# Performance work log

Hardware: AMD Instinct MI355X
Metric: run time of the kernel (lower is better)

The kernel has to match this reference:

```python
import jax, jax.numpy as jnp
import numpy as np

C_S, C_HID, H, P, V = 128, 16, 12, 4, 8
EPS = 1e-08
SOFTPLUS_INV_1 = 0.541324854612918


def _pts_from_linear(x, n_pts):
    # torch: split [..., 3*n] into 3 chunks of n, stack on dim=-1 -> [..., n, 3]
    B, N = x.shape[:2]
    return jnp.moveaxis(x.reshape(B, N, 3, n_pts), -2, -1)


def setup_inputs() -> dict:
    key = jax.random.key(0)
    ks = jax.random.split(key, 16)
    B, N = 2, 512
    hc = H * C_HID            # 192
    hpq = H * P * 3           # 144
    hpkv = H * (P + V) * 3    # 432
    cat_dim = H * (C_HID + V * 4)  # 576
    sc = 0.02
    inp = {
        "s": jax.random.normal(ks[0], (B, N, C_S), jnp.float32),
        "R": jax.random.normal(ks[1], (B, N, 3, 3), jnp.float32),
        "t": jax.random.normal(ks[2], (B, N, 3), jnp.float32),
        "pair_mask": jnp.ones((B, N, N), jnp.float32),
        "Wq": jax.random.normal(ks[3], (C_S, hc), jnp.float32) * sc,
        "bq": jnp.zeros((hc,), jnp.float32),
        "Wkv": jax.random.normal(ks[4], (C_S, 2 * hc), jnp.float32) * sc,
        "bkv": jnp.zeros((2 * hc,), jnp.float32),
        "Wqp": jax.random.normal(ks[5], (C_S, hpq), jnp.float32) * sc,
        "bqp": jnp.zeros((hpq,), jnp.float32),
        "Wkvp": jax.random.normal(ks[6], (C_S, hpkv), jnp.float32) * sc,
        "bkvp": jnp.zeros((hpkv,), jnp.float32),
        "head_weights": jnp.full((H,), SOFTPLUS_INV_1, jnp.float32),
        "Wout": jax.random.normal(ks[7], (cat_dim, C_S), jnp.float32) * sc,
        "bout": jnp.zeros((C_S,), jnp.float32),
    }
    return inp


def reference(s, R, t, pair_mask, Wq, bq, Wkv, bkv, Wqp, bqp, Wkvp, bkvp,
              head_weights, Wout, bout):
    B, N, _ = s.shape
    # scalar q/k/v
    q = (s @ Wq + bq).reshape(B, N, H, C_HID)
    kv = (s @ Wkv + bkv).reshape(B, N, H, 2 * C_HID)
    k, v = kv[..., :C_HID], kv[..., C_HID:]

    # point q/k/v in global frame: R x + t
    qp = _pts_from_linear(s @ Wqp + bqp, H * P)           # [B,N,HP,3]
    qp = jnp.einsum('bnij,bnpj->bnpi', R, qp) + t[:, :, None]
    qp = qp.reshape(B, N, H, P, 3)
    kvp = _pts_from_linear(s @ Wkvp + bkvp, H * (P + V))  # [B,N,H(P+V),3]
    kvp = jnp.einsum('bnij,bnpj->bnpi', R, kvp) + t[:, :, None]
    kvp = kvp.reshape(B, N, H, P + V, 3)
    kp, vp = kvp[..., :P, :], kvp[..., P:, :]

    # scalar attention logits [B,H,N,N]
    a = jnp.einsum('bihc,bjhc->bhij', q, k) * (1.0 / np.sqrt(3 * C_HID))

    # point-distance bias: sum_p ||q_i - k_j||^2 via |q|^2+|k|^2-2q.k
    sq_q = jnp.sum(qp * qp, axis=(-1, -2))   # [B,N,H]
    sq_k = jnp.sum(kp * kp, axis=(-1, -2))   # [B,N,H]
    cross = jnp.einsum('bihpc,bjhpc->bhij', qp, kp)
    d2 = (jnp.swapaxes(sq_q, 1, 2)[..., :, None]
          + jnp.swapaxes(sq_k, 1, 2)[..., None, :]
          - 2.0 * cross)                      # [B,H,N,N]
    hw = jax.nn.softplus(head_weights) * np.sqrt(1.0 / (3 * (P * 9.0 / 2)))
    pt_att = d2 * hw[None, :, None, None] * (-0.5)

    square_mask = 100000.0 * (pair_mask - 1.0)            # [B,N,N]
    a = jax.nn.softmax(a + pt_att + square_mask[:, None], axis=-1)

    # scalar output
    o = jnp.einsum('bhij,bjhc->bihc', a, v).reshape(B, N, H * C_HID)

    # point output, rotated back to local frame: R^T (x - t) form -> R^T x - t
    o_pt = jnp.einsum('bhij,bjhvc->bihvc', a, vp)         # [B,N,H,V,3]
    o_pt = jnp.einsum('bnji,bnhvj->bnhvi', R, o_pt) - t[:, :, None, None]
    o_pt_norm = jnp.sqrt(jnp.sum(o_pt * o_pt, axis=-1) + EPS).reshape(B, N, H * V)
    o_pt_flat = o_pt.reshape(B, N, H * V, 3)

    cat = jnp.concatenate(
        [o, o_pt_flat[..., 0], o_pt_flat[..., 1], o_pt_flat[..., 2], o_pt_norm],
        axis=-1)                                           # [B,N,576]
    return cat @ Wout + bout
```

## Files before the change

kernel.cpp:

```cpp
#include <hip/hip_runtime.h>
#include <hip/hip_bf16.h>
#include <math.h>

#define H_    12
#define B_    2
#define N_    512
#define BH_   (B_*H_)
#define QSCALE 0.14433756729740643f
#define CPT_K  0.13608276348795434f

#define OFF_WPP  1245184
#define OFF_WOP  1318912
#define OFF_BIA  1355776
#define OFF_QB   1356928
#define OFF_KP   1553536
#define OFF_VP   1750144
#define OFF_SA   2045056
#define OFF_SB   2057344
#define OFF_CATP 2069632

typedef __attribute__((ext_vector_type(8))) short sh8;
typedef __attribute__((ext_vector_type(4))) float f32x4;
typedef unsigned short u16t;

static __device__ __forceinline__ u16t f2b(float x) {
    __hip_bfloat16 h = __float2bfloat16(x);
    return *reinterpret_cast<u16t*>(&h);
}
static __device__ __forceinline__ int catp_idx(int tok, int col) {
    return (tok >> 4)*9216 + (col >> 5)*512 + ((col >> 3) & 3)*128
         + (tok & 15)*8 + (col & 7);
}

__global__ __launch_bounds__(256) void convert_kernel(
    const float* __restrict__ Wq,  const float* __restrict__ bq,
    const float* __restrict__ Wkv, const float* __restrict__ bkv,
    const float* __restrict__ Wqp, const float* __restrict__ bqp,
    const float* __restrict__ Wkvp,const float* __restrict__ bkvp,
    const float* __restrict__ Wout, float* __restrict__ ws)
{
    const int g = blockIdx.x * 256 + threadIdx.x;
    union { sh8 v; u16t u[8]; } pk;

    if (g < 18432) {
        int u = g;
        int n = u & 63, kq = (u >> 6) & 3, ks = (u >> 8) & 3, nt = u >> 10;
        int col = nt*64 + n, k0 = ks*32 + kq*8;
        const float* w; int lc, od;
        if (col < 192)      { w = Wq;   lc = col;     od = 192; }
        else if (col < 576) { w = Wkv;  lc = col-192; od = 384; }
        else if (col < 720) { w = Wqp;  lc = col-576; od = 144; }
        else                { w = Wkvp; lc = col-720; od = 432; }
        #pragma unroll
        for (int j = 0; j < 8; ++j) pk.u[j] = f2b(w[(k0+j)*od + lc]);
        *((sh8*)((u16t*)(ws + OFF_WPP)) + u) = pk.v;
    } else if (g < 27648) {
        int u = g - 18432;
        int n = u & 63, kq = (u >> 6) & 3, rem = u >> 8;
        int ks = rem % 18, nt = rem / 18;
        int col = nt*64 + n, k0 = ks*32 + kq*8;
        #pragma unroll
        for (int j = 0; j < 8; ++j) pk.u[j] = f2b(Wout[(k0+j)*128 + col]);
        *((sh8*)((u16t*)(ws + OFF_WOP)) + u) = pk.v;
    } else if (g < 28800) {
        int col = g - 27648;
        float bv;
        if (col < 192)      bv = bq[col];
        else if (col < 576) bv = bkv[col-192];
        else if (col < 720) bv = bqp[col-576];
        else                bv = bkvp[col-720];
        ws[OFF_BIA + col] = bv;
    }
}

__global__ __launch_bounds__(512) void projpack_kernel(
    const float* __restrict__ s,
    const float* __restrict__ Rg, const float* __restrict__ tg,
    const float* __restrict__ hwg, float* __restrict__ ws)
{
    __shared__ float ldsP[8][1160];

    u16t* Qb = (u16t*)(ws + OFF_QB);
    u16t* Kp = (u16t*)(ws + OFF_KP);
    u16t* Vp = (u16t*)(ws + OFF_VP);
    float* sa_g = ws + OFF_SA;
    float* sb_g = ws + OFF_SB;

    const int tid  = threadIdx.x;
    const int w    = tid >> 6, lane = tid & 63;
    const int kq   = lane >> 4, lx = lane & 15;
    const int tok0 = blockIdx.x * 8;
    const int b    = tok0 >> 9, n0 = tok0 & 511;

    sh8 afr[4];
    #pragma unroll
    for (int ks = 0; ks < 4; ++ks) {
        const float* src = s + (tok0 + (lx & 7))*128 + ks*32 + kq*8;
        float4 u0 = *(const float4*)(src);
        float4 u1 = *(const float4*)(src+4);
        union { sh8 v; u16t u[8]; } pk;
        pk.u[0]=f2b(u0.x); pk.u[1]=f2b(u0.y); pk.u[2]=f2b(u0.z); pk.u[3]=f2b(u0.w);
        pk.u[4]=f2b(u1.x); pk.u[5]=f2b(u1.y); pk.u[6]=f2b(u1.z); pk.u[7]=f2b(u1.w);
        afr[ks] = pk.v;
    }

    const sh8* Bp = (const sh8*)((const u16t*)(ws + OFF_WPP));
    const float* bias = ws + OFF_BIA;

    #pragma unroll 3
    for (int g = 0; g < 9; ++g) {
        int gg = w*9 + g;
        int nt = gg >> 2, nq = gg & 3;
        f32x4 acc = {0.f,0.f,0.f,0.f};
        #pragma unroll
        for (int ks = 0; ks < 4; ++ks) {
            sh8 bf = Bp[((nt*4 + ks)*4 + kq)*64 + nq*16 + lx];
            acc = __builtin_amdgcn_mfma_f32_16x16x32_bf16(afr[ks], bf, acc, 0, 0, 0);
        }
        float bv = bias[gg*16 + lx];
        if (kq < 2) {
            #pragma unroll
            for (int r = 0; r < 4; ++r)
                ldsP[kq*4 + r][gg*16 + lx] = acc[r] + bv;
        }
    }
    __syncthreads();

    for (int idx = tid; idx < 8*48; idx += 512) {
        int tk = idx / 48, p = idx % 48;
        int tok = tok0 + tk;
        const float* Rr = Rg + tok*9;
        const float* tr = tg + tok*3;
        float x0 = ldsP[tk][576 +  0 + p];
        float x1 = ldsP[tk][576 + 48 + p];
        float x2 = ldsP[tk][576 + 96 + p];
        ldsP[tk][576 +  0 + p] = Rr[0]*x0 + Rr[1]*x1 + Rr[2]*x2 + tr[0];
        ldsP[tk][576 + 48 + p] = Rr[3]*x0 + Rr[4]*x1 + Rr[5]*x2 + tr[1];
        ldsP[tk][576 + 96 + p] = Rr[6]*x0 + Rr[7]*x1 + Rr[8]*x2 + tr[2];
    }
    for (int idx = tid; idx < 8*144; idx += 512) {
        int tk = idx / 144, p = idx % 144;
        int tok = tok0 + tk;
        const float* Rr = Rg + tok*9;
        const float* tr = tg + tok*3;
        float x0 = ldsP[tk][720 +   0 + p];
        float x1 = ldsP[tk][720 + 144 + p];
        float x2 = ldsP[tk][720 + 288 + p];
        ldsP[tk][720 +   0 + p] = Rr[0]*x0 + Rr[1]*x1 + Rr[2]*x2 + tr[0];
        ldsP[tk][720 + 144 + p] = Rr[3]*x0 + Rr[4]*x1 + Rr[5]*x2 + tr[1];
        ldsP[tk][720 + 288 + p] = Rr[6]*x0 + Rr[7]*x1 + Rr[8]*x2 + tr[2];
    }
    __syncthreads();

    for (int idx = tid; idx < 8*24; idx += 512) {
        int tk = idx / 24, r2 = idx % 24, h = r2 >> 1, half = r2 & 1;
        float hx = hwg[h];
        float sp = (hx > 20.f) ? hx : log1pf(__expf(hx));
        float c_pt = -0.5f * sp * CPT_K;
        union { sh8 v[2]; u16t u[16]; } pk;
        if (half == 0) {
            #pragma unroll
            for (int e = 0; e < 16; ++e) pk.u[e] = f2b(ldsP[tk][h*16 + e] * QSCALE);
        } else {
            float qs = -2.f * c_pt;
            #pragma unroll
            for (int e = 0; e < 12; ++e)
                pk.u[e] = f2b(ldsP[tk][576 + (e%3)*48 + h*4 + e/3] * qs);
            pk.u[12]=0; pk.u[13]=0; pk.u[14]=0; pk.u[15]=0;
        }
        u16t* dst = Qb + ((b*H_+h)*N_ + n0 + tk)*32 + half*16;
        *(sh8*)dst = pk.v[0];
        *(sh8*)(dst+8) = pk.v[1];
    }
    for (int idx = tid; idx < 8*48; idx += 512) {
        int tk = idx / 48, r2 = idx % 48, h = r2 >> 2, fq = r2 & 3;
        int j = n0 + tk, bh = b*H_ + h;
        union { sh8 v; u16t u[8]; } pk;
        #pragma unroll
        for (int e = 0; e < 8; ++e) {
            int c = fq*8 + e;
            float val;
            if (c < 16)      val = ldsP[tk][192 + h*32 + c];
            else if (c < 28) val = ldsP[tk][720 + ((c-16)%3)*144 + h*12 + (c-16)/3];
            else             val = 0.f;
            pk.u[e] = f2b(val);
        }
        *(sh8*)(Kp + bh*16384 + (j>>4)*512 + fq*128 + (j&15)*8) = pk.v;
    }
    for (int idx = tid; idx < 480; idx += 512) {
        int h = idx / 40, d = idx % 40;
        int bh = b*H_ + h;
        union { sh8 v; u16t u[8]; } pk;
        #pragma unroll
        for (int e = 0; e < 8; ++e) {
            float val;
            if (d < 16) val = ldsP[e][192 + h*32 + 16 + d];
            else        val = ldsP[e][720 + ((d-16)%3)*144 + h*12 + 4 + (d-16)/3];
            pk.u[e] = f2b(val);
        }
        int j = n0;
        *(sh8*)(Vp + bh*24576 + (j>>5)*1536 + (d>>4)*512 + ((j>>3)&3)*128
                + (d&15)*8) = pk.v;
    }
    for (int idx = tid; idx < 8*12; idx += 512) {
        int tk = idx / 12, h = idx % 12;
        float hx = hwg[h];
        float sp = (hx > 20.f) ? hx : log1pf(__expf(hx));
        float c_pt = -0.5f * sp * CPT_K;
        float sq = 0.f, sk = 0.f;
        #pragma unroll
        for (int pp = 0; pp < 4; ++pp)
            #pragma unroll
            for (int c = 0; c < 3; ++c) {
                float a = ldsP[tk][576 + c*48  + h*4  + pp]; sq += a*a;
                float k = ldsP[tk][720 + c*144 + h*12 + pp]; sk += k*k;
            }
        sa_g[(b*H_+h)*N_ + n0 + tk] = c_pt * sq;
        sb_g[(b*H_+h)*N_ + n0 + tk] = c_pt * sk;
    }
}

__global__ __launch_bounds__(512, 2) void attn_kernel(
    const float* __restrict__ Rg, const float* __restrict__ tg,
    const float* __restrict__ maskg, float* __restrict__ ws)
{
    __shared__ u16t smP[8*16*72];
    __shared__ float mbuf[3*128*20];
    __shared__ float obuf[32*32];

    const u16t* Qb = (const u16t*)(ws + OFF_QB);
    const u16t* Kp = (const u16t*)(ws + OFF_KP);
    const u16t* Vp = (const u16t*)(ws + OFF_VP);
    const float* sa_g = ws + OFF_SA;
    const float* sb_g = ws + OFF_SB;
    u16t* catp = (u16t*)(ws + OFF_CATP);

    const int tid  = threadIdx.x;
    const int w    = tid >> 6, lane = tid & 63;
    const int rg   = w & 1, jh = w >> 1;
    const int kq   = lane >> 4, lx = lane & 15;
    const int bh   = blockIdx.x >> 4;
    const int it   = blockIdx.x & 15;
    const int b    = bh / H_, h = bh % H_;
    const int i0   = it * 32;

    sh8 qfrag = *(const sh8*)(Qb + (bh*N_ + i0 + rg*16 + lx)*32 + kq*8);
    float sa_r[4];
    #pragma unroll
    for (int r = 0; r < 4; ++r)
        sa_r[r] = sa_g[bh*N_ + i0 + rg*16 + kq*4 + r];

    float m_run[4] = {-1e30f,-1e30f,-1e30f,-1e30f};
    float l_run[4] = {0.f,0.f,0.f,0.f};
    f32x4 oc0 = {0.f,0.f,0.f,0.f}, oc1 = oc0, oc2 = oc0;

    const float* mrow = maskg + (size_t)(b*N_ + i0 + rg*16 + kq*4)*N_ + lx;
    u16t* pw = smP + w*1152;

    #pragma unroll
    for (int t = 0; t < 2; ++t) {
        const int jt = jh*2 + t;
        const int j0 = jt * 64;

        f32x4 sc[4];
        #pragma unroll
        for (int st = 0; st < 4; ++st) {
            sh8 kf = *(const sh8*)(Kp + bh*16384 + (jt*4+st)*512 + kq*128 + lx*8);
            f32x4 z = {0.f,0.f,0.f,0.f};
            sc[st] = __builtin_amdgcn_mfma_f32_16x16x32_bf16(qfrag, kf, z, 0, 0, 0);
        }
        float sbv[4];
        #pragma unroll
        for (int st = 0; st < 4; ++st) sbv[st] = sb_g[bh*N_ + j0 + st*16 + lx];
        float mb[16];
        #pragma unroll
        for (int r = 0; r < 4; ++r)
            #pragma unroll
            for (int st = 0; st < 4; ++st)
                mb[r*4+st] = mrow[r*N_ + j0 + st*16];

        float L[16];
        #pragma unroll
        for (int st = 0; st < 4; ++st)
            #pragma unroll
            for (int r = 0; r < 4; ++r)
                L[st*4+r] = sc[st][r] + sa_r[r] + sbv[st] + 1e5f*(mb[r*4+st] - 1.f);

        #pragma unroll
        for (int r = 0; r < 4; ++r) {
            float tm = fmaxf(fmaxf(L[0*4+r], L[1*4+r]), fmaxf(L[2*4+r], L[3*4+r]));
            tm = fmaxf(tm, __shfl_xor(tm, 1));
            tm = fmaxf(tm, __shfl_xor(tm, 2));
            tm = fmaxf(tm, __shfl_xor(tm, 4));
            tm = fmaxf(tm, __shfl_xor(tm, 8));
            float mnew = fmaxf(m_run[r], tm);
            float al = __expf(m_run[r] - mnew);
            m_run[r] = mnew;
            l_run[r] *= al;
            oc0[r] *= al; oc1[r] *= al; oc2[r] *= al;
        }
        #pragma unroll
        for (int st = 0; st < 4; ++st)
            #pragma unroll
            for (int r = 0; r < 4; ++r) {
                float p = __expf(L[st*4+r] - m_run[r]);
                l_run[r] += p;
                pw[(kq*4+r)*72 + st*16 + lx] = f2b(p);
            }
        #pragma unroll
        for (int c = 0; c < 2; ++c) {
            sh8 pa = *(const sh8*)(pw + lx*72 + c*32 + kq*8);
            #pragma unroll
            for (int nq = 0; nq < 3; ++nq) {
                sh8 vf = *(const sh8*)(Vp + bh*24576 + (jt*2+c)*1536 + nq*512
                                        + kq*128 + lx*8);
                if (nq == 0) oc0 = __builtin_amdgcn_mfma_f32_16x16x32_bf16(pa, vf, oc0, 0,0,0);
                if (nq == 1) oc1 = __builtin_amdgcn_mfma_f32_16x16x32_bf16(pa, vf, oc1, 0,0,0);
                if (nq == 2) oc2 = __builtin_amdgcn_mfma_f32_16x16x32_bf16(pa, vf, oc2, 0,0,0);
            }
        }
    }

    if (jh > 0) {
        float* mb = mbuf + ((jh-1)*128 + rg*64 + lane)*20;
        #pragma unroll
        for (int r = 0; r < 4; ++r) {
            mb[r]      = m_run[r];
            mb[4 + r]  = l_run[r];
            mb[8 + r]  = oc0[r];
            mb[12 + r] = oc1[r];
            mb[16 + r] = oc2[r];
        }
    }
    __syncthreads();
    if (jh == 0) {
        float linv[4];
        #pragma unroll
        for (int r = 0; r < 4; ++r) {
            float ms = m_run[r];
            #pragma unroll
            for (int q = 0; q < 3; ++q)
                ms = fmaxf(ms, mbuf[(q*128 + rg*64 + lane)*20 + r]);
            float eA = __expf(m_run[r] - ms);
            float l = l_run[r]*eA;
            oc0[r] *= eA; oc1[r] *= eA; oc2[r] *= eA;
            #pragma unroll
            for (int q = 0; q < 3; ++q) {
                const float* mb = mbuf + (q*128 + rg*64 + lane)*20;
                float e = __expf(mb[r] - ms);
                l      += mb[4+r]*e;
                oc0[r] += mb[8+r]*e;
                oc1[r] += mb[12+r]*e;
                oc2[r] += mb[16+r]*e;
            }
            l += __shfl_xor(l, 1); l += __shfl_xor(l, 2);
            l += __shfl_xor(l, 4); l += __shfl_xor(l, 8);
            linv[r] = 1.f / l;
        }

        #pragma unroll
        for (int r = 0; r < 4; ++r) {
            int tok = b*N_ + i0 + rg*16 + kq*4 + r;
            catp[catp_idx(tok, h*16 + lx)] = f2b(oc0[r] * linv[r]);
            obuf[(rg*16 + kq*4 + r)*32 + lx]      = oc1[r] * linv[r];
            obuf[(rg*16 + kq*4 + r)*32 + 16 + lx] = oc2[r] * linv[r];
        }

        #pragma unroll
        for (int tsk = 0; tsk < 2; ++tsk) {
            int task = lane + tsk*64;
            int r = task >> 3, pv = task & 7;
            int tok = b*N_ + i0 + rg*16 + r;
            const float* Rr = Rg + tok*9;
            const float* tr = tg + tok*3;
            float g0 = obuf[(rg*16 + r)*32 + pv*3 + 0];
            float g1 = obuf[(rg*16 + r)*32 + pv*3 + 1];
            float g2 = obuf[(rg*16 + r)*32 + pv*3 + 2];
            float px = Rr[0]*g0 + Rr[3]*g1 + Rr[6]*g2 - tr[0];
            float py = Rr[1]*g0 + Rr[4]*g1 + Rr[7]*g2 - tr[1];
            float pz = Rr[2]*g0 + Rr[5]*g1 + Rr[8]*g2 - tr[2];
            float nrm = sqrtf(px*px + py*py + pz*pz + 1e-8f);
            catp[catp_idx(tok, 192 + h*8 + pv)] = f2b(px);
            catp[catp_idx(tok, 288 + h*8 + pv)] = f2b(py);
            catp[catp_idx(tok, 384 + h*8 + pv)] = f2b(pz);
            catp[catp_idx(tok, 480 + h*8 + pv)] = f2b(nrm);
        }
    }
}

__global__ __launch_bounds__(512) void out_kernel(
    const float* __restrict__ bout, const float* __restrict__ ws,
    float* __restrict__ out)
{
    __shared__ float part[2][3][64][4];

    const int tid = threadIdx.x;
    const int w = tid >> 6, lane = tid & 63;
    const int cg = w & 1, kh = w >> 1;
    const int lx = lane & 15, kq = lane >> 4;
    const int nt = blockIdx.x, mt = blockIdx.y;

    const sh8* Ap = (const sh8*)((const u16t*)(ws + OFF_CATP));
    const sh8* Bp = (const sh8*)((const u16t*)(ws + OFF_WOP));

    const int ke0 = (kh*18) >> 2;
    const int ke1 = ((kh+1)*18) >> 2;

    f32x4 acc = {0.f,0.f,0.f,0.f};
    #pragma unroll 5
    for (int ks = ke0; ks < ke1; ++ks) {
        sh8 af = Ap[((mt*18 + ks)*4 + kq)*16 + lx];
        sh8 bf = Bp[(((nt>>1)*18 + ks)*4 + kq)*64 + (nt&1)*32 + cg*16 + lx];
        acc = __builtin_amdgcn_mfma_f32_16x16x32_bf16(af, bf, acc, 0, 0, 0);
    }
    if (kh > 0) {
        #pragma unroll
        for (int r = 0; r < 4; ++r) part[cg][kh-1][lane][r] = acc[r];
    }
    __syncthreads();
    if (kh == 0) {
        int col = nt*32 + cg*16 + lx;
        float bv = bout[col];
        #pragma unroll
        for (int r = 0; r < 4; ++r) {
            int row = mt*16 + kq*4 + r;
            out[row*128 + col] = acc[r] + part[cg][0][lane][r]
                               + part[cg][1][lane][r] + part[cg][2][lane][r] + bv;
        }
    }
}

extern "C" void kernel_launch(void* const* d_in, const int* in_sizes, int n_in,
                              void* d_out, int out_size, void* d_ws, size_t ws_size,
                              hipStream_t stream) {
    const float* s    = (const float*)d_in[0];
    const float* R    = (const float*)d_in[1];
    const float* t    = (const float*)d_in[2];
    const float* mask = (const float*)d_in[3];
    const float* Wq   = (const float*)d_in[4];
    const float* bq   = (const float*)d_in[5];
    const float* Wkv  = (const float*)d_in[6];
    const float* bkv  = (const float*)d_in[7];
    const float* Wqp  = (const float*)d_in[8];
    const float* bqp  = (const float*)d_in[9];
    const float* Wkvp = (const float*)d_in[10];
    const float* bkvp = (const float*)d_in[11];
    const float* hw   = (const float*)d_in[12];
    const float* Wout = (const float*)d_in[13];
    const float* bout = (const float*)d_in[14];
    float* ws  = (float*)d_ws;
    float* out = (float*)d_out;

    convert_kernel<<<113, 256, 0, stream>>>(Wq, bq, Wkv, bkv,
                                            Wqp, bqp, Wkvp, bkvp, Wout, ws);
    projpack_kernel<<<128, 512, 0, stream>>>(s, R, t, hw, ws);
    attn_kernel<<<BH_*16, 512, 0, stream>>>(R, t, mask, ws);
    out_kernel<<<dim3(4, 64), 512, 0, stream>>>(bout, ws, out);
}
```

Measured before the change: 109.8 us.

## Fuse weight bf16 conversion into projection and output kernels, split projection grid

Measured after the change: 108.4 us. About the same (-1.2%).

```diff
diff --git a/kernel.cpp b/kernel.cpp
--- a/kernel.cpp
+++ b/kernel.cpp
@@ -9,9 +9,6 @@
 #define QSCALE 0.14433756729740643f
 #define CPT_K  0.13608276348795434f
 
-#define OFF_WPP  1245184
-#define OFF_WOP  1318912
-#define OFF_BIA  1355776
 #define OFF_QB   1356928
 #define OFF_KP   1553536
 #define OFF_VP   1750144
@@ -32,51 +29,15 @@
          + (tok & 15)*8 + (col & 7);
 }
 
-__global__ __launch_bounds__(256) void convert_kernel(
+__global__ __launch_bounds__(512) void projpack_kernel(
+    const float* __restrict__ s,
+    const float* __restrict__ Rg, const float* __restrict__ tg,
+    const float* __restrict__ hwg,
     const float* __restrict__ Wq,  const float* __restrict__ bq,
     const float* __restrict__ Wkv, const float* __restrict__ bkv,
     const float* __restrict__ Wqp, const float* __restrict__ bqp,
     const float* __restrict__ Wkvp,const float* __restrict__ bkvp,
-    const float* __restrict__ Wout, float* __restrict__ ws)
-{
-    const int g = blockIdx.x * 256 + threadIdx.x;
-    union { sh8 v; u16t u[8]; } pk;
-
-    if (g < 18432) {
-        int u = g;
-        int n = u & 63, kq = (u >> 6) & 3, ks = (u >> 8) & 3, nt = u >> 10;
-        int col = nt*64 + n, k0 = ks*32 + kq*8;
-        const float* w; int lc, od;
-        if (col < 192)      { w = Wq;   lc = col;     od = 192; }
-        else if (col < 576) { w = Wkv;  lc = col-192; od = 384; }
-        else if (col < 720) { w = Wqp;  lc = col-576; od = 144; }
-        else                { w = Wkvp; lc = col-720; od = 432; }
-        #pragma unroll
-        for (int j = 0; j < 8; ++j) pk.u[j] = f2b(w[(k0+j)*od + lc]);
-        *((sh8*)((u16t*)(ws + OFF_WPP)) + u) = pk.v;
-    } else if (g < 27648) {
-        int u = g - 18432;
-        int n = u & 63, kq = (u >> 6) & 3, rem = u >> 8;
-        int ks = rem % 18, nt = rem / 18;
-        int col = nt*64 + n, k0 = ks*32 + kq*8;
-        #pragma unroll
-        for (int j = 0; j < 8; ++j) pk.u[j] = f2b(Wout[(k0+j)*128 + col]);
-        *((sh8*)((u16t*)(ws + OFF_WOP)) + u) = pk.v;
-    } else if (g < 28800) {
-        int col = g - 27648;
-        float bv;
-        if (col < 192)      bv = bq[col];
-        else if (col < 576) bv = bkv[col-192];
-        else if (col < 720) bv = bqp[col-576];
-        else                bv = bkvp[col-720];
-        ws[OFF_BIA + col] = bv;
-    }
-}
-
-__global__ __launch_bounds__(512) void projpack_kernel(
-    const float* __restrict__ s,
-    const float* __restrict__ Rg, const float* __restrict__ tg,
-    const float* __restrict__ hwg, float* __restrict__ ws)
+    float* __restrict__ ws)
 {
     __shared__ float ldsP[8][1160];
 
@@ -89,7 +50,8 @@
     const int tid  = threadIdx.x;
     const int w    = tid >> 6, lane = tid & 63;
     const int kq   = lane >> 4, lx = lane & 15;
-    const int tok0 = blockIdx.x * 8;
+    const int half = blockIdx.x & 1;
+    const int tok0 = (blockIdx.x >> 1) * 8;
     const int b    = tok0 >> 9, n0 = tok0 & 511;
 
     sh8 afr[4];
@@ -104,20 +66,27 @@
         afr[ks] = pk.v;
     }
 
-    const sh8* Bp = (const sh8*)((const u16t*)(ws + OFF_WPP));
-    const float* bias = ws + OFF_BIA;
-
-    #pragma unroll 3
-    for (int g = 0; g < 9; ++g) {
-        int gg = w*9 + g;
-        int nt = gg >> 2, nq = gg & 3;
+    const int gstart = (w < 4) ? w*5 : 20 + (w-4)*4;
+    const int ng     = (w < 4) ? 5 : 4;
+
+    for (int g = 0; g < ng; ++g) {
+        int gg  = half*36 + gstart + g;
+        int col = gg*16 + lx;
+        const float* wsrc; int lc, od; float bv;
+        if (col < 192)      { wsrc = Wq;   lc = col;     od = 192; bv = bq[lc]; }
+        else if (col < 576) { wsrc = Wkv;  lc = col-192; od = 384; bv = bkv[lc]; }
+        else if (col < 720) { wsrc = Wqp;  lc = col-576; od = 144; bv = bqp[lc]; }
+        else                { wsrc = Wkvp; lc = col-720; od = 432; bv = bkvp[lc]; }
+
         f32x4 acc = {0.f,0.f,0.f,0.f};
         #pragma unroll
         for (int ks = 0; ks < 4; ++ks) {
-            sh8 bf = Bp[((nt*4 + ks)*4 + kq)*64 + nq*16 + lx];
-            acc = __builtin_amdgcn_mfma_f32_16x16x32_bf16(afr[ks], bf, acc, 0, 0, 0);
-        }
-        float bv = bias[gg*16 + lx];
+            int k0 = ks*32 + kq*8;
+            union { sh8 v; u16t u[8]; } pk;
+            #pragma unroll
+            for (int j = 0; j < 8; ++j) pk.u[j] = f2b(wsrc[(k0+j)*od + lc]);
+            acc = __builtin_amdgcn_mfma_f32_16x16x32_bf16(afr[ks], pk.v, acc, 0, 0, 0);
+        }
         if (kq < 2) {
             #pragma unroll
             for (int r = 0; r < 4; ++r)
@@ -126,97 +95,118 @@
     }
     __syncthreads();
 
-    for (int idx = tid; idx < 8*48; idx += 512) {
-        int tk = idx / 48, p = idx % 48;
-        int tok = tok0 + tk;
-        const float* Rr = Rg + tok*9;
-        const float* tr = tg + tok*3;
-        float x0 = ldsP[tk][576 +  0 + p];
-        float x1 = ldsP[tk][576 + 48 + p];
-        float x2 = ldsP[tk][576 + 96 + p];
-        ldsP[tk][576 +  0 + p] = Rr[0]*x0 + Rr[1]*x1 + Rr[2]*x2 + tr[0];
-        ldsP[tk][576 + 48 + p] = Rr[3]*x0 + Rr[4]*x1 + Rr[5]*x2 + tr[1];
-        ldsP[tk][576 + 96 + p] = Rr[6]*x0 + Rr[7]*x1 + Rr[8]*x2 + tr[2];
-    }
-    for (int idx = tid; idx < 8*144; idx += 512) {
-        int tk = idx / 144, p = idx % 144;
-        int tok = tok0 + tk;
-        const float* Rr = Rg + tok*9;
-        const float* tr = tg + tok*3;
-        float x0 = ldsP[tk][720 +   0 + p];
-        float x1 = ldsP[tk][720 + 144 + p];
-        float x2 = ldsP[tk][720 + 288 + p];
-        ldsP[tk][720 +   0 + p] = Rr[0]*x0 + Rr[1]*x1 + Rr[2]*x2 + tr[0];
-        ldsP[tk][720 + 144 + p] = Rr[3]*x0 + Rr[4]*x1 + Rr[5]*x2 + tr[1];
-        ldsP[tk][720 + 288 + p] = Rr[6]*x0 + Rr[7]*x1 + Rr[8]*x2 + tr[2];
-    }
-    __syncthreads();
-
-    for (int idx = tid; idx < 8*24; idx += 512) {
-        int tk = idx / 24, r2 = idx % 24, h = r2 >> 1, half = r2 & 1;
-        float hx = hwg[h];
-        float sp = (hx > 20.f) ? hx : log1pf(__expf(hx));
-        float c_pt = -0.5f * sp * CPT_K;
-        union { sh8 v[2]; u16t u[16]; } pk;
-        if (half == 0) {
-            #pragma unroll
-            for (int e = 0; e < 16; ++e) pk.u[e] = f2b(ldsP[tk][h*16 + e] * QSCALE);
-        } else {
-            float qs = -2.f * c_pt;
+    if (half == 1) {
+        for (int idx = tid; idx < 8*48; idx += 512) {
+            int tk = idx / 48, p = idx % 48;
+            int tok = tok0 + tk;
+            const float* Rr = Rg + tok*9;
+            const float* tr = tg + tok*3;
+            float x0 = ldsP[tk][576 +  0 + p];
+            float x1 = ldsP[tk][576 + 48 + p];
+            float x2 = ldsP[tk][576 + 96 + p];
+            ldsP[tk][576 +  0 + p] = Rr[0]*x0 + Rr[1]*x1 + Rr[2]*x2 + tr[0];
+            ldsP[tk][576 + 48 + p] = Rr[3]*x0 + Rr[4]*x1 + Rr[5]*x2 + tr[1];
+            ldsP[tk][576 + 96 + p] = Rr[6]*x0 + Rr[7]*x1 + Rr[8]*x2 + tr[2];
+        }
+        for (int idx = tid; idx < 8*144; idx += 512) {
+            int tk = idx / 144, p = idx % 144;
+            int tok = tok0 + tk;
+            const float* Rr = Rg + tok*9;
+            const float* tr = tg + tok*3;
+            float x0 = ldsP[tk][720 +   0 + p];
+            float x1 = ldsP[tk][720 + 144 + p];
+            float x2 = ldsP[tk][720 + 288 + p];
+            ldsP[tk][720 +   0 + p] = Rr[0]*x0 + Rr[1]*x1 + Rr[2]*x2 + tr[0];
+            ldsP[tk][720 + 144 + p] = Rr[3]*x0 + Rr[4]*x1 + Rr[5]*x2 + tr[1];
+            ldsP[tk][720 + 288 + p] = Rr[6]*x0 + Rr[7]*x1 + Rr[8]*x2 + tr[2];
+        }
+        __syncthreads();
+
+        for (int idx = tid; idx < 8*12; idx += 512) {
+            int tk = idx / 12, h = idx % 12;
+            float hx = hwg[h];
+            float sp = (hx > 20.f) ? hx : log1pf(__expf(hx));
+            float qs = sp * CPT_K;
+            union { sh8 v[2]; u16t u[16]; } pk;
             #pragma unroll
             for (int e = 0; e < 12; ++e)
                 pk.u[e] = f2b(ldsP[tk][576 + (e%3)*48 + h*4 + e/3] * qs);
             pk.u[12]=0; pk.u[13]=0; pk.u[14]=0; pk.u[15]=0;
-        }
-        u16t* dst = Qb + ((b*H_+h)*N_ + n0 + tk)*32 + half*16;
-        *(sh8*)dst = pk.v[0];
-        *(sh8*)(dst+8) = pk.v[1];
-    }
-    for (int idx = tid; idx < 8*48; idx += 512) {
-        int tk = idx / 48, r2 = idx % 48, h = r2 >> 2, fq = r2 & 3;
-        int j = n0 + tk, bh = b*H_ + h;
-        union { sh8 v; u16t u[8]; } pk;
-        #pragma unroll
-        for (int e = 0; e < 8; ++e) {
-            int c = fq*8 + e;
-            float val;
-            if (c < 16)      val = ldsP[tk][192 + h*32 + c];
-            else if (c < 28) val = ldsP[tk][720 + ((c-16)%3)*144 + h*12 + (c-16)/3];
-            else             val = 0.f;
-            pk.u[e] = f2b(val);
-        }
-        *(sh8*)(Kp + bh*16384 + (j>>4)*512 + fq*128 + (j&15)*8) = pk.v;
-    }
-    for (int idx = tid; idx < 480; idx += 512) {
-        int h = idx / 40, d = idx % 40;
-        int bh = b*H_ + h;
-        union { sh8 v; u16t u[8]; } pk;
-        #pragma unroll
-        for (int e = 0; e < 8; ++e) {
-            float val;
-            if (d < 16) val = ldsP[e][192 + h*32 + 16 + d];
-            else        val = ldsP[e][720 + ((d-16)%3)*144 + h*12 + 4 + (d-16)/3];
-            pk.u[e] = f2b(val);
-        }
-        int j = n0;
-        *(sh8*)(Vp + bh*24576 + (j>>5)*1536 + (d>>4)*512 + ((j>>3)&3)*128
-                + (d&15)*8) = pk.v;
-    }
-    for (int idx = tid; idx < 8*12; idx += 512) {
-        int tk = idx / 12, h = idx % 12;
-        float hx = hwg[h];
-        float sp = (hx > 20.f) ? hx : log1pf(__expf(hx));
-        float c_pt = -0.5f * sp * CPT_K;
-        float sq = 0.f, sk = 0.f;
-        #pragma unroll
-        for (int pp = 0; pp < 4; ++pp)
-            #pragma unroll
-            for (int c = 0; c < 3; ++c) {
-                float a = ldsP[tk][576 + c*48  + h*4  + pp]; sq += a*a;
-                float k = ldsP[tk][720 + c*144 + h*12 + pp]; sk += k*k;
+            u16t* dst = Qb + ((b*H_+h)*N_ + n0 + tk)*32 + 16;
+            *(sh8*)dst = pk.v[0];
+            *(sh8*)(dst+8) = pk.v[1];
+        }
+        for (int idx = tid; idx < 8*24; idx += 512) {
+            int tk = idx / 24, r2 = idx % 24, h = r2 >> 1, fq = 2 + (r2 & 1);
+            int j = n0 + tk, bh = b*H_ + h;
+            union { sh8 v; u16t u[8]; } pk;
+            #pragma unroll
+            for (int e = 0; e < 8; ++e) {
+                int c = fq*8 + e;
+                float val;
+                if (c < 28) val = ldsP[tk][720 + ((c-16)%3)*144 + h*12 + (c-16)/3];
+                else        val = 0.f;
+                pk.u[e] = f2b(val);
             }
-        sa_g[(b*H_+h)*N_ + n0 + tk] = c_pt * sq;
-        sb_g[(b*H_+h)*N_ + n0 + tk] = c_pt * sk;
+            *(sh8*)(Kp + bh*16384 + (j>>4)*512 + fq*128 + (j&15)*8) = pk.v;
+        }
+        for (int idx = tid; idx < 12*24; idx += 512) {
+            int h = idx / 24, d = 16 + idx % 24;
+            int bh = b*H_ + h;
+            union { sh8 v; u16t u[8]; } pk;
+            #pragma unroll
+            for (int e = 0; e < 8; ++e)
+                pk.u[e] = f2b(ldsP[e][720 + ((d-16)%3)*144 + h*12 + 4 + (d-16)/3]);
+            int j = n0;
+            *(sh8*)(Vp + bh*24576 + (j>>5)*1536 + (d>>4)*512 + ((j>>3)&3)*128
+                    + (d&15)*8) = pk.v;
+        }
+        for (int idx = tid; idx < 8*12; idx += 512) {
+            int tk = idx / 12, h = idx % 12;
+            float hx = hwg[h];
+            float sp = (hx > 20.f) ? hx : log1pf(__expf(hx));
+            float c_pt = -0.5f * sp * CPT_K;
+            float sq = 0.f, sk = 0.f;
+            #pragma unroll
+            for (int pp = 0; pp < 4; ++pp)
+                #pragma unroll
+                for (int c = 0; c < 3; ++c) {
+                    float a = ldsP[tk][576 + c*48  + h*4  + pp]; sq += a*a;
+                    float k = ldsP[tk][720 + c*144 + h*12 + pp]; sk += k*k;
+                }
+            sa_g[(b*H_+h)*N_ + n0 + tk] = c_pt * sq;
+            sb_g[(b*H_+h)*N_ + n0 + tk] = c_pt * sk;
+        }
+    } else {
+        for (int idx = tid; idx < 8*12; idx += 512) {
+            int tk = idx / 12, h = idx % 12;
+            union { sh8 v[2]; u16t u[16]; } pk;
+            #pragma unroll
+            for (int e = 0; e < 16; ++e) pk.u[e] = f2b(ldsP[tk][h*16 + e] * QSCALE);
+            u16t* dst = Qb + ((b*H_+h)*N_ + n0 + tk)*32;
+            *(sh8*)dst = pk.v[0];
+            *(sh8*)(dst+8) = pk.v[1];
+        }
+        for (int idx = tid; idx < 8*24; idx += 512) {
+            int tk = idx / 24, r2 = idx % 24, h = r2 >> 1, fq = r2 & 1;
+            int j = n0 + tk, bh = b*H_ + h;
+            union { sh8 v; u16t u[8]; } pk;
+            #pragma unroll
+            for (int e = 0; e < 8; ++e)
+                pk.u[e] = f2b(ldsP[tk][192 + h*32 + fq*8 + e]);
+            *(sh8*)(Kp + bh*16384 + (j>>4)*512 + fq*128 + (j&15)*8) = pk.v;
+        }
+        for (int idx = tid; idx < 12*16; idx += 512) {
+            int h = idx / 16, d = idx % 16;
+            int bh = b*H_ + h;
+            union { sh8 v; u16t u[8]; } pk;
+            #pragma unroll
+            for (int e = 0; e < 8; ++e)
+                pk.u[e] = f2b(ldsP[e][192 + h*32 + 16 + d]);
+            int j = n0;
+            *(sh8*)(Vp + bh*24576 + (j>>5)*1536 + (d>>4)*512 + ((j>>3)&3)*128
+                    + (d&15)*8) = pk.v;
+        }
     }
 }
 
@@ -389,8 +379,8 @@
 }
 
 __global__ __launch_bounds__(512) void out_kernel(
-    const float* __restrict__ bout, const float* __restrict__ ws,
-    float* __restrict__ out)
+    const float* __restrict__ Wout, const float* __restrict__ bout,
+    const float* __restrict__ ws, float* __restrict__ out)
 {
     __shared__ float part[2][3][64][4];
 
@@ -401,8 +391,8 @@
     const int nt = blockIdx.x, mt = blockIdx.y;
 
     const sh8* Ap = (const sh8*)((const u16t*)(ws + OFF_CATP));
-    const sh8* Bp = (const sh8*)((const u16t*)(ws + OFF_WOP));
-
+
+    const int col = nt*32 + cg*16 + lx;
     const int ke0 = (kh*18) >> 2;
     const int ke1 = ((kh+1)*18) >> 2;
 
@@ -410,8 +400,11 @@
     #pragma unroll 5
     for (int ks = ke0; ks < ke1; ++ks) {
         sh8 af = Ap[((mt*18 + ks)*4 + kq)*16 + lx];
-        sh8 bf = Bp[(((nt>>1)*18 + ks)*4 + kq)*64 + (nt&1)*32 + cg*16 + lx];
-        acc = __builtin_amdgcn_mfma_f32_16x16x32_bf16(af, bf, acc, 0, 0, 0);
+        int k0 = ks*32 + kq*8;
+        union { sh8 v; u16t u[8]; } pk;
+        #pragma unroll
+        for (int j = 0; j < 8; ++j) pk.u[j] = f2b(Wout[(k0+j)*128 + col]);
+        acc = __builtin_amdgcn_mfma_f32_16x16x32_bf16(af, pk.v, acc, 0, 0, 0);
     }
     if (kh > 0) {
         #pragma unroll
@@ -419,7 +412,6 @@
     }
     __syncthreads();
     if (kh == 0) {
-        int col = nt*32 + cg*16 + lx;
         float bv = bout[col];
         #pragma unroll
         for (int r = 0; r < 4; ++r) {
@@ -451,9 +443,8 @@
     float* ws  = (float*)d_ws;
     float* out = (float*)d_out;
 
-    convert_kernel<<<113, 256, 0, stream>>>(Wq, bq, Wkv, bkv,
-                                            Wqp, bqp, Wkvp, bkvp, Wout, ws);
-    projpack_kernel<<<128, 512, 0, stream>>>(s, R, t, hw, ws);
+    projpack_kernel<<<256, 512, 0, stream>>>(s, R, t, hw, Wq, bq, Wkv, bkv,
+                                             Wqp, bqp, Wkvp, bkvp, ws);
     attn_kernel<<<BH_*16, 512, 0, stream>>>(R, t, mask, ws);
-    out_kernel<<<dim3(4, 64), 512, 0, stream>>>(bout, ws, out);
-}
+    out_kernel<<<dim3(4, 64), 512, 0, stream>>>(Wout, bout, ws, out);
+}
```
